# Kernel tuning notes

Hardware: AMD Instinct MI355X
Metric: run time of the kernel (lower is better)

Reference implementation:

```python
import jax, jax.numpy as jnp
import numpy as np

N, H, L = 128, 2, 1024  # nodes, heads, sequence (input_dim)


def setup_inputs() -> dict:
    key = jax.random.key(0)
    k1, k2 = jax.random.split(key)
    x = jax.random.normal(k1, (N, H, L), dtype=jnp.float32)
    Amat = jax.random.normal(k2, (N, N), dtype=jnp.float32)
    taus = jnp.ones((N, H), dtype=jnp.float32) * 6.2       # as in __init__
    R0dTaus = jnp.ones((N, H), dtype=jnp.float32) * 1.35   # as in __init__
    return {"x": x, "Amat": Amat, "taus": taus, "R0dTaus": R0dTaus}


def reference(x, Amat, taus, R0dTaus):
    n, h, l = x.shape
    idx = jnp.arange(l)
    mask = (idx[:, None] >= idx[None, :])                      # causal lower-tri
    # temporal lag matrix: mat[i,j] = i-j for j<=i else 0 (matches create_temporal_mat)
    mat = jnp.where(mask, (idx[:, None] - idx[None, :]).astype(jnp.float32), 0.0)
    maskf = mask.astype(jnp.float32)

    tempAmat = Amat.T + jnp.eye(n, dtype=x.dtype)              # (n, n)
    signal = jax.nn.relu(x)                                    # (n, h, l)
    Ss = 1.0 - jnp.cumsum(signal, axis=-1)                     # (n, h, l)

    # IsMat[n,h,i,j] = exp((i-j) * log(1 - 1/tau[n,h])) on the causal band
    decay = jnp.log(1.0 - 1.0 / taus)                          # (n, h)
    IsMat = jnp.exp(mat[None, None] * decay[..., None, None]) * maskf  # (n,h,l,l)
    Is = jnp.einsum('nhij,nhj->nhi', IsMat, signal)            # causal decay matvec

    alpha = 1.0 - jnp.exp(-R0dTaus[..., None] * Is)            # (n, h, l)
    # Alpha[k,h,l] = sum_m tempAmat[m,k] * alpha[m,h,l]  (avoids (n,n,h,l) temp)
    Alpha = jnp.einsum('mk,mhl->khl', tempAmat, alpha)
    predSignal = Alpha * Ss
    return (predSignal, signal, tempAmat.T)
```

## Files before the change

### kernel.cpp

```cpp
#include <hip/hip_runtime.h>
#include <hip/hip_bf16.h>

#define NN 128
#define HH 2
#define LL 1024
#define NH (NN * HH)
#define NHL (NN * HH * LL)
#define COLS (HH * LL)

__global__ __launch_bounds__(256) void row_scan_kernel(
    const float* __restrict__ x, const float* __restrict__ taus,
    const float* __restrict__ r0d, float* __restrict__ out_signal,
    float* __restrict__ ws_alpha, float* __restrict__ ws_ss) {
  const int row = blockIdx.x;
  const int tid = threadIdx.x;

  const float4* xr = (const float4*)(x + (size_t)row * LL);
  float4 v = xr[tid];
  float s0 = fmaxf(v.x, 0.f);
  float s1 = fmaxf(v.y, 0.f);
  float s2 = fmaxf(v.z, 0.f);
  float s3 = fmaxf(v.w, 0.f);

  const float tau = taus[row];
  const float d = 1.f - 1.f / tau;
  const float R0 = r0d[row];

  float c0 = s0, c1 = c0 + s1, c2 = c1 + s2, c3 = c2 + s3;
  float l0 = s0;
  float l1 = fmaf(d, l0, s1);
  float l2 = fmaf(d, l1, s2);
  float l3 = fmaf(d, l2, s3);

  __shared__ float ssum[256];
  __shared__ float sis[256];

  float vs = c3;
  float vi = l3;
  ssum[tid] = vs;
  sis[tid] = vi;

  float D = d * d;
  D = D * D;
  float Dp = D;
  for (int off = 1; off < 256; off <<= 1) {
    __syncthreads();
    float ps = (tid >= off) ? ssum[tid - off] : 0.f;
    float pi = (tid >= off) ? sis[tid - off] : 0.f;
    __syncthreads();
    vs += ps;
    vi = fmaf(Dp, pi, vi);
    ssum[tid] = vs;
    sis[tid] = vi;
    Dp *= Dp;
  }
  __syncthreads();
  const float exs = (tid > 0) ? ssum[tid - 1] : 0.f;
  const float exi = (tid > 0) ? sis[tid - 1] : 0.f;

  float cum0 = exs + c0, cum1 = exs + c1, cum2 = exs + c2, cum3 = exs + c3;
  float is0 = fmaf(d, exi, s0);
  float is1 = fmaf(d, is0, s1);
  float is2 = fmaf(d, is1, s2);
  float is3 = fmaf(d, is2, s3);

  float4 sig = make_float4(s0, s1, s2, s3);
  float4 ss = make_float4(1.f - cum0, 1.f - cum1, 1.f - cum2, 1.f - cum3);
  float4 al = make_float4(1.f - __expf(-R0 * is0), 1.f - __expf(-R0 * is1),
                          1.f - __expf(-R0 * is2), 1.f - __expf(-R0 * is3));

  const size_t base = (size_t)row * LL / 4 + tid;
  ((float4*)(out_signal))[base] = sig;
  ((float4*)(ws_alpha))[base] = al;
  ((float4*)(ws_ss))[base] = ss;
}

__global__ __launch_bounds__(256) void mix_kernel(
    const float* __restrict__ Amat, const float* __restrict__ ws_alpha,
    const float* __restrict__ ws_ss, float* __restrict__ pred,
    float* __restrict__ tmatT) {
  const int idx = blockIdx.x * 256 + threadIdx.x;
  const int k = idx >> 11;
  const int col = idx & (COLS - 1);

  const float* __restrict__ acol = ws_alpha + col;
  const float* __restrict__ arow = Amat + k * NN;
  float acc = ws_alpha[(size_t)k * COLS + col];
#pragma unroll 8
  for (int m = 0; m < NN; ++m) {
    acc = fmaf(arow[m], acol[(size_t)m * COLS], acc);
  }
  pred[idx] = acc * ws_ss[idx];

  if (idx < NN * NN) {
    const int kk = idx >> 7;
    const int mm = idx & (NN - 1);
    tmatT[idx] = Amat[idx] + (kk == mm ? 1.f : 0.f);
  }
}

extern "C" void kernel_launch(void* const* d_in, const int* in_sizes, int n_in,
                              void* d_out, int out_size, void* d_ws,
                              size_t ws_size, hipStream_t stream) {
  const float* x = (const float*)d_in[0];
  const float* Amat = (const float*)d_in[1];
  const float* taus = (const float*)d_in[2];
  const float* r0d = (const float*)d_in[3];

  float* out = (float*)d_out;
  float* out_pred = out;
  float* out_signal = out + NHL;
  float* out_tmatT = out + 2 * NHL;

  float* ws = (float*)d_ws;
  float* ws_alpha = ws;
  float* ws_ss = ws + NHL;

  row_scan_kernel<<<NH, 256, 0, stream>>>(x, taus, r0d, out_signal, ws_alpha,
                                          ws_ss);
  mix_kernel<<<NHL / 256, 256, 0, stream>>>(Amat, ws_alpha, ws_ss, out_pred,
                                            out_tmatT);
}
```

Before: 71.23 us.

## Use wave shuffles for scan and register-block mix over four output rows

```diff
diff --git a/kernel.cpp b/kernel.cpp
--- a/kernel.cpp
+++ b/kernel.cpp
@@ -14,6 +14,8 @@
     float* __restrict__ ws_alpha, float* __restrict__ ws_ss) {
   const int row = blockIdx.x;
   const int tid = threadIdx.x;
+  const int lane = tid & 63;
+  const int wave = tid >> 6;
 
   const float4* xr = (const float4*)(x + (size_t)row * LL);
   float4 v = xr[tid];
@@ -32,34 +34,47 @@
   float l2 = fmaf(d, l1, s2);
   float l3 = fmaf(d, l2, s3);
 
-  __shared__ float ssum[256];
-  __shared__ float sis[256];
-
   float vs = c3;
   float vi = l3;
-  ssum[tid] = vs;
-  sis[tid] = vi;
-
   float D = d * d;
   D = D * D;
   float Dp = D;
-  for (int off = 1; off < 256; off <<= 1) {
-    __syncthreads();
-    float ps = (tid >= off) ? ssum[tid - off] : 0.f;
-    float pi = (tid >= off) ? sis[tid - off] : 0.f;
-    __syncthreads();
-    vs += ps;
-    vi = fmaf(Dp, pi, vi);
-    ssum[tid] = vs;
-    sis[tid] = vi;
+#pragma unroll
+  for (int off = 1; off < 64; off <<= 1) {
+    float ps = __shfl_up(vs, off);
+    float pi = __shfl_up(vi, off);
+    if (lane >= off) {
+      vs += ps;
+      vi = fmaf(Dp, pi, vi);
+    }
     Dp *= Dp;
   }
+
+  __shared__ float tw_s[4];
+  __shared__ float tw_i[4];
+  if (lane == 63) {
+    tw_s[wave] = vs;
+    tw_i[wave] = vi;
+  }
   __syncthreads();
-  const float exs = (tid > 0) ? ssum[tid - 1] : 0.f;
-  const float exi = (tid > 0) ? sis[tid - 1] : 0.f;
+
+  float S_in = 0.f, I_in = 0.f;
+  for (int u = 0; u < wave; ++u) {
+    S_in += tw_s[u];
+    I_in = fmaf(I_in, Dp, tw_i[u]);
+  }
+
+  float es = __shfl_up(vs, 1);
+  float ei = __shfl_up(vi, 1);
+  if (lane == 0) {
+    es = 0.f;
+    ei = 0.f;
+  }
+  const float exs = S_in + es;
+  const float state = fmaf(I_in, exp2f((float)lane * log2f(D)), ei);
 
   float cum0 = exs + c0, cum1 = exs + c1, cum2 = exs + c2, cum3 = exs + c3;
-  float is0 = fmaf(d, exi, s0);
+  float is0 = fmaf(d, state, s0);
   float is1 = fmaf(d, is0, s1);
   float is2 = fmaf(d, is1, s2);
   float is3 = fmaf(d, is2, s3);
@@ -79,23 +94,51 @@
     const float* __restrict__ Amat, const float* __restrict__ ws_alpha,
     const float* __restrict__ ws_ss, float* __restrict__ pred,
     float* __restrict__ tmatT) {
-  const int idx = blockIdx.x * 256 + threadIdx.x;
-  const int k = idx >> 11;
-  const int col = idx & (COLS - 1);
+  const int bid = blockIdx.x;
+  const int tid = threadIdx.x;
+  const int rg = bid >> 3;
+  const int cg = bid & 7;
+  const int col = (cg << 8) + tid;
+  const int k0 = __builtin_amdgcn_readfirstlane(rg << 2);
 
-  const float* __restrict__ acol = ws_alpha + col;
-  const float* __restrict__ arow = Amat + k * NN;
-  float acc = ws_alpha[(size_t)k * COLS + col];
+  const float* __restrict__ a0 = Amat + (k0 + 0) * NN;
+  const float* __restrict__ a1 = Amat + (k0 + 1) * NN;
+  const float* __restrict__ a2 = Amat + (k0 + 2) * NN;
+  const float* __restrict__ a3 = Amat + (k0 + 3) * NN;
+
+  float acc0 = ws_alpha[(size_t)(k0 + 0) * COLS + col];
+  float acc1 = ws_alpha[(size_t)(k0 + 1) * COLS + col];
+  float acc2 = ws_alpha[(size_t)(k0 + 2) * COLS + col];
+  float acc3 = ws_alpha[(size_t)(k0 + 3) * COLS + col];
+
+  const float* __restrict__ ac = ws_alpha + col;
 #pragma unroll 8
   for (int m = 0; m < NN; ++m) {
-    acc = fmaf(arow[m], acol[(size_t)m * COLS], acc);
+    const float av = ac[(size_t)m * COLS];
+    acc0 = fmaf(a0[m], av, acc0);
+    acc1 = fmaf(a1[m], av, acc1);
+    acc2 = fmaf(a2[m], av, acc2);
+    acc3 = fmaf(a3[m], av, acc3);
   }
-  pred[idx] = acc * ws_ss[idx];
 
-  if (idx < NN * NN) {
-    const int kk = idx >> 7;
-    const int mm = idx & (NN - 1);
-    tmatT[idx] = Amat[idx] + (kk == mm ? 1.f : 0.f);
+  pred[(size_t)(k0 + 0) * COLS + col] =
+      acc0 * ws_ss[(size_t)(k0 + 0) * COLS + col];
+  pred[(size_t)(k0 + 1) * COLS + col] =
+      acc1 * ws_ss[(size_t)(k0 + 1) * COLS + col];
+  pred[(size_t)(k0 + 2) * COLS + col] =
+      acc2 * ws_ss[(size_t)(k0 + 2) * COLS + col];
+  pred[(size_t)(k0 + 3) * COLS + col] =
+      acc3 * ws_ss[(size_t)(k0 + 3) * COLS + col];
+
+  const int fid = bid * 256 + tid;
+  if (fid < NN * NN / 4) {
+    float4 t = ((const float4*)Amat)[fid];
+    const int e = fid << 2;
+    if (((e + 0) % (NN + 1)) == 0) t.x += 1.f;
+    if (((e + 1) % (NN + 1)) == 0) t.y += 1.f;
+    if (((e + 2) % (NN + 1)) == 0) t.z += 1.f;
+    if (((e + 3) % (NN + 1)) == 0) t.w += 1.f;
+    ((float4*)tmatT)[fid] = t;
   }
 }
 
@@ -118,6 +161,6 @@
 
   row_scan_kernel<<<NH, 256, 0, stream>>>(x, taus, r0d, out_signal, ws_alpha,
                                           ws_ss);
-  mix_kernel<<<NHL / 256, 256, 0, stream>>>(Amat, ws_alpha, ws_ss, out_pred,
-                                            out_tmatT);
+  mix_kernel<<<256, 256, 0, stream>>>(Amat, ws_alpha, ws_ss, out_pred,
+                                      out_tmatT);
 }
```

After: 68.86 us. -3.3%, faster.
